# Kernel optimization log

Hardware: AMD Instinct MI355X
Metric: run time of the kernel (lower is better)

The kernel has to match this reference:

```python
import jax, jax.numpy as jnp
import numpy as np

B, H, S, DH = 2, 16, 2048, 64
MASK_FILL = -10000.0


def setup_inputs() -> dict:
    key = jax.random.key(0)
    kq, kk, kv = jax.random.split(key, 3)
    q = jax.random.normal(kq, (B, H, S, DH), dtype=jnp.float32)
    k = jax.random.normal(kk, (B, H, S, DH), dtype=jnp.float32)
    v = jax.random.normal(kv, (B, H, S, DH), dtype=jnp.float32)
    # causal mask: True where attention is disallowed (upper triangle)
    mask = jnp.triu(jnp.ones((S, S), dtype=jnp.bool_), k=1)
    return {"q": q, "k": k, "v": v, "mask": mask}


def reference(q, k, v, mask):
    scale = 1.0 / jnp.sqrt(jnp.asarray(k.shape[-1], dtype=q.dtype))
    # scores: [B, H, S_q, S_k]
    scores = jnp.einsum("bhqd,bhkd->bhqk", q, k) * scale
    # additive mask: masked_fill on a zeros [S_k, S_v] matrix -> -10000 where mask
    attn_bias = jnp.where(mask, jnp.asarray(MASK_FILL, dtype=k.dtype),
                          jnp.asarray(0.0, dtype=k.dtype))
    scores = scores + attn_bias  # broadcast over batch/heads
    attn = jax.nn.softmax(scores, axis=-1)
    # dropout_rate = 0.0 -> identity
    return jnp.einsum("bhqk,bhkd->bhqd", attn, v)
```

## Files before the change

kernel.cpp:

```cpp
#include <hip/hip_runtime.h>


#define S_LEN  2048
#define DHDIM  64
#define NHEADS 32
#define LDP    72
#define M2     23.083120654223414f
#define QSCALE 0.18033688011117658f

typedef __attribute__((ext_vector_type(8))) short bf16x8;
typedef __attribute__((ext_vector_type(4))) float f32x4;

__device__ __forceinline__ unsigned short f2bf(float f) {
    unsigned u = __float_as_uint(f);
    return (unsigned short)((u + 0x7fffu + ((u >> 16) & 1u)) >> 16);
}
__device__ __forceinline__ void ld8(const float* p, float* f) {
    float4 a = *(const float4*)p, b = *(const float4*)(p + 4);
    f[0]=a.x; f[1]=a.y; f[2]=a.z; f[3]=a.w; f[4]=b.x; f[5]=b.y; f[6]=b.z; f[7]=b.w;
}
__device__ __forceinline__ uint4 pack8(const float* f, float scale) {
    union { uint4 v; unsigned short s[8]; } w;
    #pragma unroll
    for (int j = 0; j < 8; j++) w.s[j] = f2bf(f[j] * scale);
    return w.v;
}
__device__ __forceinline__ unsigned packhi(float a, float b) {
#if __has_builtin(__builtin_amdgcn_perm)
    return __builtin_amdgcn_perm(__float_as_uint(b), __float_as_uint(a), 0x07060302u);
#else
    return (__float_as_uint(a) >> 16) | (__float_as_uint(b) & 0xffff0000u);
#endif
}

__global__ __launch_bounds__(256) void prep(
    const float* __restrict__ Qf, const float* __restrict__ Kf,
    const float* __restrict__ Vf, unsigned short* __restrict__ qb,
    unsigned short* __restrict__ kb, unsigned short* __restrict__ vtb)
{
    const int st = blockIdx.x, bh = blockIdx.y;
    __shared__ unsigned short lt[64][LDP];
    const float* vp = Vf + ((size_t)bh * S_LEN + st * 64) * DHDIM;
    for (int c = threadIdx.x; c < 512; c += 256) {
        int s = c >> 3, d0 = (c & 7) * 8;
        float f[8]; ld8(vp + s * DHDIM + d0, f);
        #pragma unroll
        for (int j = 0; j < 8; j++) lt[d0 + j][s] = f2bf(f[j]);
    }
    size_t off = ((size_t)(bh * 32 + st) * 4096) + (size_t)threadIdx.x * 16;
    float f[8];
    ld8(Qf + off, f);     *(uint4*)(qb + off)     = pack8(f, QSCALE);
    ld8(Qf + off + 8, f); *(uint4*)(qb + off + 8) = pack8(f, QSCALE);
    ld8(Kf + off, f);     *(uint4*)(kb + off)     = pack8(f, 1.0f);
    ld8(Kf + off + 8, f); *(uint4*)(kb + off + 8) = pack8(f, 1.0f);
    __syncthreads();
    unsigned short* op = vtb + (size_t)bh * DHDIM * S_LEN + st * 64;
    for (int c = threadIdx.x; c < 512; c += 256) {
        int d = c >> 3, s0 = (c & 7) * 8;
        *(uint4*)(op + (size_t)d * S_LEN + s0) = *(const uint4*)&lt[d][s0];
    }
}

__global__ __launch_bounds__(256) void fattn_splitk(
    const unsigned short* __restrict__ Qp, const unsigned short* __restrict__ Kp,
    const unsigned short* __restrict__ Vp,
    float* __restrict__ pO, float* __restrict__ pL)
{
    __shared__ unsigned short smem[192 * LDP];
    unsigned short (*ks)[LDP]  = (unsigned short(*)[LDP])smem;
    unsigned short (*vts)[LDP] = (unsigned short(*)[LDP])(smem + 64 * LDP);
    unsigned short (*qs)[LDP]  = (unsigned short(*)[LDP])(smem + 128 * LDP);
    unsigned short (*pst)[LDP] = qs;

    const int id   = blockIdx.y * 64 + blockIdx.x;
    const int qt   = 31 - (id >> 6);
    const int rem  = id & 63;
    const int bh   = rem >> 1;
    const int half = rem & 1;
    const int kmid = (qt + 2) >> 1;
    const int k0   = half ? kmid : 0;
    const int k1   = half ? qt + 1 : kmid;
    const int slot = ((bh * 32 + qt) << 1) | half;

    const int tid = threadIdx.x;
    const int wave = tid >> 6, lane = tid & 63;
    const int quad = lane >> 4, l16 = lane & 15;

    {
        const unsigned short* src = Qp + ((size_t)bh * S_LEN + qt * 64) * DHDIM;
        for (int c = tid; c < 512; c += 256) {
            int row = c >> 3, c8 = (c & 7) * 8;
            *(uint4*)&qs[row][c8] = *(const uint4*)(src + row * DHDIM + c8);
        }
    }
    __syncthreads();

    const int prow = wave * 16 + l16;
    const bf16x8 bq0 = *(const bf16x8*)&qs[prow][quad * 8];
    const bf16x8 bq1 = *(const bf16x8*)&qs[prow][32 + quad * 8];

    float l_p = 0.f;
    f32x4 of[4];
    #pragma unroll
    for (int n = 0; n < 4; n++) of[n] = (f32x4){0.f, 0.f, 0.f, 0.f};

    for (int kt = k0; kt < k1; kt++) {
        __syncthreads();

        const unsigned short* ksrc = Kp + ((size_t)bh * S_LEN + kt * 64) * DHDIM;
        const unsigned short* vsrc = Vp + (size_t)bh * DHDIM * S_LEN + kt * 64;
        for (int c = tid; c < 512; c += 256) {
            int row = c >> 3, c8 = (c & 7) * 8;
            *(uint4*)&ks[row][c8]  = *(const uint4*)(ksrc + row * DHDIM + c8);
            *(uint4*)&vts[row][c8] = *(const uint4*)(vsrc + (size_t)row * S_LEN + c8);
        }
        __syncthreads();

        f32x4 sf[4];
        #pragma unroll
        for (int n = 0; n < 4; n++) {
            bf16x8 ak0 = *(const bf16x8*)&ks[n * 16 + l16][quad * 8];
            bf16x8 ak1 = *(const bf16x8*)&ks[n * 16 + l16][32 + quad * 8];
            sf[n] = (f32x4){-M2, -M2, -M2, -M2};
            sf[n] = __builtin_amdgcn_mfma_f32_16x16x32_bf16(ak0, bq0, sf[n], 0, 0, 0);
            sf[n] = __builtin_amdgcn_mfma_f32_16x16x32_bf16(ak1, bq1, sf[n], 0, 0, 0);
        }

        const bool diag = (kt == qt);
        #pragma unroll
        for (int n = 0; n < 4; n++) {
            float p[4];
            #pragma unroll
            for (int r = 0; r < 4; r++) {
                p[r] = exp2f(sf[n][r]);
                if (diag && (n * 16 + quad * 4 + r > prow)) p[r] = 0.f;
                l_p += p[r];
            }
            uint2 dw;
            dw.x = packhi(p[0], p[1]);
            dw.y = packhi(p[2], p[3]);
            *(uint2*)&pst[prow][n * 16 + quad * 4] = dw;
        }
        asm volatile("s_waitcnt lgkmcnt(0)" ::: "memory");

        bf16x8 bp0 = *(const bf16x8*)&pst[prow][quad * 8];
        bf16x8 bp1 = *(const bf16x8*)&pst[prow][32 + quad * 8];
        #pragma unroll
        for (int n = 0; n < 4; n++) {
            bf16x8 av0 = *(const bf16x8*)&vts[n * 16 + l16][quad * 8];
            bf16x8 av1 = *(const bf16x8*)&vts[n * 16 + l16][32 + quad * 8];
            of[n] = __builtin_amdgcn_mfma_f32_16x16x32_bf16(av0, bp0, of[n], 0, 0, 0);
            of[n] = __builtin_amdgcn_mfma_f32_16x16x32_bf16(av1, bp1, of[n], 0, 0, 0);
        }
    }

    l_p += __shfl_xor(l_p, 16);
    l_p += __shfl_xor(l_p, 32);
    if (quad == 0) pL[slot * 64 + prow] = l_p;
    float* op = pO + (size_t)slot * 4096 + prow * 64;
    #pragma unroll
    for (int n = 0; n < 4; n++)
        *(float4*)(op + n * 16 + quad * 4) =
            make_float4(of[n][0], of[n][1], of[n][2], of[n][3]);
}

__global__ __launch_bounds__(256) void combine(
    const float* __restrict__ pO, const float* __restrict__ pL,
    float* __restrict__ O)
{
    const int qt = blockIdx.x, bh = blockIdx.y;
    const int sa = ((bh * 32 + qt) << 1), sb = sa | 1;
    const float* A = pO + (size_t)sa * 4096;
    const float* B = pO + (size_t)sb * 4096;
    float* out = O + ((size_t)bh * S_LEN + qt * 64) * DHDIM;
    #pragma unroll
    for (int k = 0; k < 4; k++) {
        int c = threadIdx.x + k * 256;
        int row = c >> 4;
        float inv = 1.f / (pL[sa * 64 + row] + pL[sb * 64 + row]);
        float4 a = *(const float4*)(A + c * 4);
        float4 b = *(const float4*)(B + c * 4);
        *(float4*)(out + c * 4) = make_float4(
            (a.x + b.x) * inv, (a.y + b.y) * inv,
            (a.z + b.z) * inv, (a.w + b.w) * inv);
    }
}

template <bool PRE>
__global__ __launch_bounds__(256) void fattn_kernel(
    const void* __restrict__ Qp, const void* __restrict__ Kp,
    const void* __restrict__ Vp, float* __restrict__ O)
{
    __shared__ unsigned short smem[192 * LDP];
    unsigned short (*ks)[LDP]  = (unsigned short(*)[LDP])smem;
    unsigned short (*vts)[LDP] = (unsigned short(*)[LDP])(smem + 64 * LDP);
    unsigned short (*qs)[LDP]  = (unsigned short(*)[LDP])(smem + 128 * LDP);
    unsigned short (*pst)[LDP] = qs;

    const int id = blockIdx.y * 32 + blockIdx.x;
    const int g  = id >> 8;
    const int r8 = id & 255;
    const int bh = r8 >> 3;
    const int s8 = r8 & 7;
    const int qt = (g == 0) ? 31 - 2 * s8 : (g == 1) ? 2 * s8
                 : (g == 2) ? 30 - 2 * s8 : 2 * s8 + 1;

    const int tid = threadIdx.x;
    const int wave = tid >> 6, lane = tid & 63;
    const int quad = lane >> 4, l16 = lane & 15;

    if constexpr (PRE) {
        const unsigned short* src = (const unsigned short*)Qp
            + ((size_t)bh * S_LEN + qt * 64) * DHDIM;
        for (int c = tid; c < 512; c += 256) {
            int row = c >> 3, c8 = (c & 7) * 8;
            *(uint4*)&qs[row][c8] = *(const uint4*)(src + row * DHDIM + c8);
        }
    } else {
        const float* src = (const float*)Qp + ((size_t)bh * S_LEN + qt * 64) * DHDIM;
        for (int c = tid; c < 512; c += 256) {
            int row = c >> 3, c8 = (c & 7) * 8;
            float f[8]; ld8(src + row * DHDIM + c8, f);
            *(uint4*)&qs[row][c8] = pack8(f, QSCALE);
        }
    }
    __syncthreads();

    const int prow = wave * 16 + l16;
    const bf16x8 bq0 = *(const bf16x8*)&qs[prow][quad * 8];
    const bf16x8 bq1 = *(const bf16x8*)&qs[prow][32 + quad * 8];

    float l_p = 0.f;
    f32x4 of[4];
    #pragma unroll
    for (int n = 0; n < 4; n++) of[n] = (f32x4){0.f, 0.f, 0.f, 0.f};

    for (int kt = 0; kt <= qt; kt++) {
        __syncthreads();
        if constexpr (PRE) {
            const unsigned short* ksrc = (const unsigned short*)Kp
                + ((size_t)bh * S_LEN + kt * 64) * DHDIM;
            const unsigned short* vsrc = (const unsigned short*)Vp
                + (size_t)bh * DHDIM * S_LEN + kt * 64;
            for (int c = tid; c < 512; c += 256) {
                int row = c >> 3, c8 = (c & 7) * 8;
                *(uint4*)&ks[row][c8]  = *(const uint4*)(ksrc + row * DHDIM + c8);
                *(uint4*)&vts[row][c8] = *(const uint4*)(vsrc + (size_t)row * S_LEN + c8);
            }
        } else {
            const float* ksrc = (const float*)Kp + ((size_t)bh * S_LEN + kt * 64) * DHDIM;
            const float* vsrc = (const float*)Vp + ((size_t)bh * S_LEN + kt * 64) * DHDIM;
            for (int c = tid; c < 512; c += 256) {
                int row = c >> 3, c8 = (c & 7) * 8;
                float f[8];
                ld8(ksrc + row * DHDIM + c8, f);
                *(uint4*)&ks[row][c8] = pack8(f, 1.0f);
                ld8(vsrc + row * DHDIM + c8, f);
                #pragma unroll
                for (int j = 0; j < 8; j++) vts[c8 + j][row] = f2bf(f[j]);
            }
        }
        __syncthreads();

        f32x4 sf[4];
        #pragma unroll
        for (int n = 0; n < 4; n++) {
            bf16x8 ak0 = *(const bf16x8*)&ks[n * 16 + l16][quad * 8];
            bf16x8 ak1 = *(const bf16x8*)&ks[n * 16 + l16][32 + quad * 8];
            sf[n] = (f32x4){-M2, -M2, -M2, -M2};
            sf[n] = __builtin_amdgcn_mfma_f32_16x16x32_bf16(ak0, bq0, sf[n], 0, 0, 0);
            sf[n] = __builtin_amdgcn_mfma_f32_16x16x32_bf16(ak1, bq1, sf[n], 0, 0, 0);
        }

        const bool diag = (kt == qt);
        #pragma unroll
        for (int n = 0; n < 4; n++) {
            float p[4];
            #pragma unroll
            for (int r = 0; r < 4; r++) {
                p[r] = exp2f(sf[n][r]);
                if (diag && (n * 16 + quad * 4 + r > prow)) p[r] = 0.f;
                l_p += p[r];
            }
            uint2 dw;
            dw.x = packhi(p[0], p[1]);
            dw.y = packhi(p[2], p[3]);
            *(uint2*)&pst[prow][n * 16 + quad * 4] = dw;
        }
        asm volatile("s_waitcnt lgkmcnt(0)" ::: "memory");

        bf16x8 bp0 = *(const bf16x8*)&pst[prow][quad * 8];
        bf16x8 bp1 = *(const bf16x8*)&pst[prow][32 + quad * 8];
        #pragma unroll
        for (int n = 0; n < 4; n++) {
            bf16x8 av0 = *(const bf16x8*)&vts[n * 16 + l16][quad * 8];
            bf16x8 av1 = *(const bf16x8*)&vts[n * 16 + l16][32 + quad * 8];
            of[n] = __builtin_amdgcn_mfma_f32_16x16x32_bf16(av0, bp0, of[n], 0, 0, 0);
            of[n] = __builtin_amdgcn_mfma_f32_16x16x32_bf16(av1, bp1, of[n], 0, 0, 0);
        }
    }

    l_p += __shfl_xor(l_p, 16);
    l_p += __shfl_xor(l_p, 32);
    const float inv = 1.f / l_p;
    float* op = O + ((size_t)bh * S_LEN + qt * 64 + prow) * DHDIM;
    #pragma unroll
    for (int n = 0; n < 4; n++)
        *(float4*)(op + n * 16 + quad * 4) = make_float4(
            of[n][0] * inv, of[n][1] * inv, of[n][2] * inv, of[n][3] * inv);
}

extern "C" void kernel_launch(void* const* d_in, const int* in_sizes, int n_in,
                              void* d_out, int out_size, void* d_ws, size_t ws_size,
                              hipStream_t stream) {
    const float* Q = (const float*)d_in[0];
    const float* K = (const float*)d_in[1];
    const float* V = (const float*)d_in[2];
    float* O = (float*)d_out;
    const size_t N = (size_t)NHEADS * S_LEN * DHDIM;
    const size_t prepB  = 3 * N * sizeof(unsigned short);
    const size_t partB  = (size_t)2048 * (4096 + 64) * sizeof(float);

    if (d_ws && ws_size >= prepB + partB) {
        unsigned short* qb  = (unsigned short*)d_ws;
        unsigned short* kb  = qb + N;
        unsigned short* vtb = kb + N;
        float* pO = (float*)((char*)d_ws + prepB);
        float* pL = pO + (size_t)2048 * 4096;
        prep<<<dim3(S_LEN / 64, NHEADS), 256, 0, stream>>>(Q, K, V, qb, kb, vtb);
        fattn_splitk<<<dim3(64, 32), 256, 0, stream>>>(qb, kb, vtb, pO, pL);
        combine<<<dim3(32, 32), 256, 0, stream>>>(pO, pL, O);
    } else if (d_ws && ws_size >= prepB) {
        unsigned short* qb  = (unsigned short*)d_ws;
        unsigned short* kb  = qb + N;
        unsigned short* vtb = kb + N;
        prep<<<dim3(S_LEN / 64, NHEADS), 256, 0, stream>>>(Q, K, V, qb, kb, vtb);
        fattn_kernel<true><<<dim3(32, 32), 256, 0, stream>>>(qb, kb, vtb, O);
    } else {
        fattn_kernel<false><<<dim3(32, 32), 256, 0, stream>>>(Q, K, V, O);
    }
}
```

Baseline: 149.3 us.

## Fuse split-K combine into attention via atomic pairing, MFMA row sums, swizzled transpose

Removes the separate combine kernel. The second of each pair of split-K blocks to finish waits on a ready flag and merges the partial output directly, and the flags are reset inside the prep kernel. The row sum of P is now computed with an extra MFMA against a ones vector instead of scalar adds and shuffles. Two further changes: exp2f is replaced by the hardware exp2 builtin, and the V transpose in prep uses an XOR-swizzled LDS layout to avoid bank conflicts. The spin-wait depends on the partner block being resident or already finished, which adds a risk of stalls.

```diff
diff --git a/kernel.cpp b/kernel.cpp
--- a/kernel.cpp
+++ b/kernel.cpp
@@ -11,6 +11,13 @@
 typedef __attribute__((ext_vector_type(8))) short bf16x8;
 typedef __attribute__((ext_vector_type(4))) float f32x4;
 
+__device__ __forceinline__ float fast_exp2(float x) {
+#if __has_builtin(__builtin_amdgcn_exp2f)
+    return __builtin_amdgcn_exp2f(x);
+#else
+    return exp2f(x);
+#endif
+}
 __device__ __forceinline__ unsigned short f2bf(float f) {
     unsigned u = __float_as_uint(f);
     return (unsigned short)((u + 0x7fffu + ((u >> 16) & 1u)) >> 16);
@@ -36,16 +43,23 @@
 __global__ __launch_bounds__(256) void prep(
     const float* __restrict__ Qf, const float* __restrict__ Kf,
     const float* __restrict__ Vf, unsigned short* __restrict__ qb,
-    unsigned short* __restrict__ kb, unsigned short* __restrict__ vtb)
+    unsigned short* __restrict__ kb, unsigned short* __restrict__ vtb,
+    int* __restrict__ flags)
 {
     const int st = blockIdx.x, bh = blockIdx.y;
+    if (flags && threadIdx.x < 2)
+        flags[threadIdx.x * 1024 + bh * 32 + st] = 0;
     __shared__ unsigned short lt[64][LDP];
     const float* vp = Vf + ((size_t)bh * S_LEN + st * 64) * DHDIM;
     for (int c = threadIdx.x; c < 512; c += 256) {
         int s = c >> 3, d0 = (c & 7) * 8;
         float f[8]; ld8(vp + s * DHDIM + d0, f);
         #pragma unroll
-        for (int j = 0; j < 8; j++) lt[d0 + j][s] = f2bf(f[j]);
+        for (int j = 0; j < 8; j++) {
+            int d = d0 + j;
+            int col = (s & 7) | ((((s >> 3) ^ (d >> 3)) & 7) << 3);
+            lt[d][col] = f2bf(f[j]);
+        }
     }
     size_t off = ((size_t)(bh * 32 + st) * 4096) + (size_t)threadIdx.x * 16;
     float f[8];
@@ -56,17 +70,20 @@
     __syncthreads();
     unsigned short* op = vtb + (size_t)bh * DHDIM * S_LEN + st * 64;
     for (int c = threadIdx.x; c < 512; c += 256) {
-        int d = c >> 3, s0 = (c & 7) * 8;
-        *(uint4*)(op + (size_t)d * S_LEN + s0) = *(const uint4*)&lt[d][s0];
+        int d = c >> 3, q = c & 7;
+        int colc = ((q ^ (d >> 3)) & 7) << 3;
+        *(uint4*)(op + (size_t)d * S_LEN + q * 8) = *(const uint4*)&lt[d][colc];
     }
 }
 
 __global__ __launch_bounds__(256) void fattn_splitk(
     const unsigned short* __restrict__ Qp, const unsigned short* __restrict__ Kp,
     const unsigned short* __restrict__ Vp,
-    float* __restrict__ pO, float* __restrict__ pL)
+    float* __restrict__ pO, float* __restrict__ pL,
+    int* __restrict__ flags, float* __restrict__ O)
 {
     __shared__ unsigned short smem[192 * LDP];
+    __shared__ int s_old;
     unsigned short (*ks)[LDP]  = (unsigned short(*)[LDP])smem;
     unsigned short (*vts)[LDP] = (unsigned short(*)[LDP])(smem + 64 * LDP);
     unsigned short (*qs)[LDP]  = (unsigned short(*)[LDP])(smem + 128 * LDP);
@@ -80,7 +97,8 @@
     const int kmid = (qt + 2) >> 1;
     const int k0   = half ? kmid : 0;
     const int k1   = half ? qt + 1 : kmid;
-    const int slot = ((bh * 32 + qt) << 1) | half;
+    const int pair = bh * 32 + qt;
+    const int slot = (pair << 1) | half;
 
     const int tid = threadIdx.x;
     const int wave = tid >> 6, lane = tid & 63;
@@ -99,8 +117,12 @@
     const bf16x8 bq0 = *(const bf16x8*)&qs[prow][quad * 8];
     const bf16x8 bq1 = *(const bf16x8*)&qs[prow][32 + quad * 8];
 
-    float l_p = 0.f;
+    bf16x8 ones;
+    #pragma unroll
+    for (int j = 0; j < 8; j++) ones[j] = (short)0x3F80;
+
     f32x4 of[4];
+    f32x4 of_l = (f32x4){0.f, 0.f, 0.f, 0.f};
     #pragma unroll
     for (int n = 0; n < 4; n++) of[n] = (f32x4){0.f, 0.f, 0.f, 0.f};
 
@@ -132,9 +154,8 @@
             float p[4];
             #pragma unroll
             for (int r = 0; r < 4; r++) {
-                p[r] = exp2f(sf[n][r]);
+                p[r] = fast_exp2(sf[n][r]);
                 if (diag && (n * 16 + quad * 4 + r > prow)) p[r] = 0.f;
-                l_p += p[r];
             }
             uint2 dw;
             dw.x = packhi(p[0], p[1]);
@@ -145,6 +166,8 @@
 
         bf16x8 bp0 = *(const bf16x8*)&pst[prow][quad * 8];
         bf16x8 bp1 = *(const bf16x8*)&pst[prow][32 + quad * 8];
+        of_l = __builtin_amdgcn_mfma_f32_16x16x32_bf16(ones, bp0, of_l, 0, 0, 0);
+        of_l = __builtin_amdgcn_mfma_f32_16x16x32_bf16(ones, bp1, of_l, 0, 0, 0);
         #pragma unroll
         for (int n = 0; n < 4; n++) {
             bf16x8 av0 = *(const bf16x8*)&vts[n * 16 + l16][quad * 8];
@@ -154,35 +177,42 @@
         }
     }
 
-    l_p += __shfl_xor(l_p, 16);
-    l_p += __shfl_xor(l_p, 32);
-    if (quad == 0) pL[slot * 64 + prow] = l_p;
-    float* op = pO + (size_t)slot * 4096 + prow * 64;
-    #pragma unroll
-    for (int n = 0; n < 4; n++)
-        *(float4*)(op + n * 16 + quad * 4) =
-            make_float4(of[n][0], of[n][1], of[n][2], of[n][3]);
-}
-
-__global__ __launch_bounds__(256) void combine(
-    const float* __restrict__ pO, const float* __restrict__ pL,
-    float* __restrict__ O)
-{
-    const int qt = blockIdx.x, bh = blockIdx.y;
-    const int sa = ((bh * 32 + qt) << 1), sb = sa | 1;
-    const float* A = pO + (size_t)sa * 4096;
-    const float* B = pO + (size_t)sb * 4096;
-    float* out = O + ((size_t)bh * S_LEN + qt * 64) * DHDIM;
-    #pragma unroll
-    for (int k = 0; k < 4; k++) {
-        int c = threadIdx.x + k * 256;
-        int row = c >> 4;
-        float inv = 1.f / (pL[sa * 64 + row] + pL[sb * 64 + row]);
-        float4 a = *(const float4*)(A + c * 4);
-        float4 b = *(const float4*)(B + c * 4);
-        *(float4*)(out + c * 4) = make_float4(
-            (a.x + b.x) * inv, (a.y + b.y) * inv,
-            (a.z + b.z) * inv, (a.w + b.w) * inv);
+    int* cnt = flags;
+    int* rdy = flags + 1024;
+    if (tid == 0) s_old = atomicAdd(&cnt[pair], 1);
+    __syncthreads();
+
+    if (s_old == 0) {
+        if (quad == 0) pL[slot * 64 + prow] = of_l[0];
+        float* op = pO + (size_t)slot * 4096 + prow * 64;
+        #pragma unroll
+        for (int n = 0; n < 4; n++)
+            *(float4*)(op + n * 16 + quad * 4) =
+                make_float4(of[n][0], of[n][1], of[n][2], of[n][3]);
+        __threadfence();
+        __syncthreads();
+        if (tid == 0)
+            __hip_atomic_store(&rdy[pair], 1, __ATOMIC_RELEASE,
+                               __HIP_MEMORY_SCOPE_AGENT);
+    } else {
+        if (tid == 0) {
+            while (__hip_atomic_load(&rdy[pair], __ATOMIC_ACQUIRE,
+                                     __HIP_MEMORY_SCOPE_AGENT) == 0)
+                __builtin_amdgcn_s_sleep(2);
+        }
+        __syncthreads();
+        __threadfence();
+        const int pslot = slot ^ 1;
+        const float inv = 1.f / (of_l[0] + pL[pslot * 64 + prow]);
+        const float* pp = pO + (size_t)pslot * 4096 + prow * 64;
+        float* op = O + ((size_t)bh * S_LEN + qt * 64 + prow) * DHDIM;
+        #pragma unroll
+        for (int n = 0; n < 4; n++) {
+            float4 a = *(const float4*)(pp + n * 16 + quad * 4);
+            *(float4*)(op + n * 16 + quad * 4) = make_float4(
+                (of[n][0] + a.x) * inv, (of[n][1] + a.y) * inv,
+                (of[n][2] + a.z) * inv, (of[n][3] + a.w) * inv);
+        }
     }
 }
 
@@ -278,7 +308,7 @@
             float p[4];
             #pragma unroll
             for (int r = 0; r < 4; r++) {
-                p[r] = exp2f(sf[n][r]);
+                p[r] = fast_exp2(sf[n][r]);
                 if (diag && (n * 16 + quad * 4 + r > prow)) p[r] = 0.f;
                 l_p += p[r];
             }
@@ -320,21 +350,22 @@
     const size_t N = (size_t)NHEADS * S_LEN * DHDIM;
     const size_t prepB  = 3 * N * sizeof(unsigned short);
     const size_t partB  = (size_t)2048 * (4096 + 64) * sizeof(float);
-
-    if (d_ws && ws_size >= prepB + partB) {
+    const size_t flagB  = 2048 * sizeof(int);
+
+    if (d_ws && ws_size >= prepB + partB + flagB) {
         unsigned short* qb  = (unsigned short*)d_ws;
         unsigned short* kb  = qb + N;
         unsigned short* vtb = kb + N;
         float* pO = (float*)((char*)d_ws + prepB);
         float* pL = pO + (size_t)2048 * 4096;
-        prep<<<dim3(S_LEN / 64, NHEADS), 256, 0, stream>>>(Q, K, V, qb, kb, vtb);
-        fattn_splitk<<<dim3(64, 32), 256, 0, stream>>>(qb, kb, vtb, pO, pL);
-        combine<<<dim3(32, 32), 256, 0, stream>>>(pO, pL, O);
+        int* flags = (int*)((char*)d_ws + prepB + partB);
+        prep<<<dim3(S_LEN / 64, NHEADS), 256, 0, stream>>>(Q, K, V, qb, kb, vtb, flags);
+        fattn_splitk<<<dim3(64, 32), 256, 0, stream>>>(qb, kb, vtb, pO, pL, flags, O);
     } else if (d_ws && ws_size >= prepB) {
         unsigned short* qb  = (unsigned short*)d_ws;
         unsigned short* kb  = qb + N;
         unsigned short* vtb = kb + N;
-        prep<<<dim3(S_LEN / 64, NHEADS), 256, 0, stream>>>(Q, K, V, qb, kb, vtb);
+        prep<<<dim3(S_LEN / 64, NHEADS), 256, 0, stream>>>(Q, K, V, qb, kb, vtb, nullptr);
         fattn_kernel<true><<<dim3(32, 32), 256, 0, stream>>>(qb, kb, vtb, O);
     } else {
         fattn_kernel<false><<<dim3(32, 32), 256, 0, stream>>>(Q, K, V, O);
```

After: 431.0 us. +188.6%, slower.

## Split only long query tiles, compute row sums via MFMA, swizzle transpose LDS

Applied to the files above, without the earlier changes.

The split-K attention now splits only query tiles 16-31 into two halves. Short tiles are processed whole and written straight to the output, and a constant table orders the work blocks from longest to shortest. The softmax denominator is accumulated with an extra MFMA against a ones vector instead of scalar adds and cross-lane shuffles, and exp2 uses the hardware builtin. The prep kernel's V transpose uses an XOR-swizzled LDS layout to reduce bank conflicts. Together these cut the number of combine tiles and the partial-result traffic, at the cost of table-driven scheduling and an extra MFMA per tile.

```diff
diff --git a/kernel.cpp b/kernel.cpp
--- a/kernel.cpp
+++ b/kernel.cpp
@@ -11,6 +11,26 @@
 typedef __attribute__((ext_vector_type(8))) short bf16x8;
 typedef __attribute__((ext_vector_type(4))) float f32x4;
 
+__device__ __constant__ unsigned char T_QT[48] = {
+    31,31,30,15, 30,29,29,28,14, 28,27,27,26,13, 26,25,25,24,12,
+    24,23,23,22,11, 22,21,21,20,10, 20,19,19,18,9, 18,17,17,16,8,
+    16,7, 6,5,4,3,2,1,0};
+__device__ __constant__ unsigned char T_K0[48] = {
+    0,16,0,0, 16,0,15,0,0, 15,0,14,0,0, 14,0,13,0,0,
+    13,0,12,0,0, 12,0,11,0,0, 11,0,10,0,0, 10,0,9,0,0,
+    9,0, 0,0,0,0,0,0,0};
+__device__ __constant__ unsigned char T_K1[48] = {
+    16,32,16,16, 31,15,30,15,15, 29,14,28,14,14, 27,13,26,13,13,
+    25,12,24,12,12, 23,11,22,11,11, 21,10,20,10,10, 19,9,18,9,9,
+    17,8, 7,6,5,4,3,2,1};
+
+__device__ __forceinline__ float fast_exp2(float x) {
+#if __has_builtin(__builtin_amdgcn_exp2f)
+    return __builtin_amdgcn_exp2f(x);
+#else
+    return exp2f(x);
+#endif
+}
 __device__ __forceinline__ unsigned short f2bf(float f) {
     unsigned u = __float_as_uint(f);
     return (unsigned short)((u + 0x7fffu + ((u >> 16) & 1u)) >> 16);
@@ -45,7 +65,11 @@
         int s = c >> 3, d0 = (c & 7) * 8;
         float f[8]; ld8(vp + s * DHDIM + d0, f);
         #pragma unroll
-        for (int j = 0; j < 8; j++) lt[d0 + j][s] = f2bf(f[j]);
+        for (int j = 0; j < 8; j++) {
+            int d = d0 + j;
+            int col = (s & 7) | ((((s >> 3) ^ (d >> 3)) & 7) << 3);
+            lt[d][col] = f2bf(f[j]);
+        }
     }
     size_t off = ((size_t)(bh * 32 + st) * 4096) + (size_t)threadIdx.x * 16;
     float f[8];
@@ -56,15 +80,16 @@
     __syncthreads();
     unsigned short* op = vtb + (size_t)bh * DHDIM * S_LEN + st * 64;
     for (int c = threadIdx.x; c < 512; c += 256) {
-        int d = c >> 3, s0 = (c & 7) * 8;
-        *(uint4*)(op + (size_t)d * S_LEN + s0) = *(const uint4*)&lt[d][s0];
+        int d = c >> 3, q = c & 7;
+        int colc = ((q ^ (d >> 3)) & 7) << 3;
+        *(uint4*)(op + (size_t)d * S_LEN + q * 8) = *(const uint4*)&lt[d][colc];
     }
 }
 
 __global__ __launch_bounds__(256) void fattn_splitk(
     const unsigned short* __restrict__ Qp, const unsigned short* __restrict__ Kp,
     const unsigned short* __restrict__ Vp,
-    float* __restrict__ pO, float* __restrict__ pL)
+    float* __restrict__ pO, float* __restrict__ pL, float* __restrict__ O)
 {
     __shared__ unsigned short smem[192 * LDP];
     unsigned short (*ks)[LDP]  = (unsigned short(*)[LDP])smem;
@@ -72,15 +97,12 @@
     unsigned short (*qs)[LDP]  = (unsigned short(*)[LDP])(smem + 128 * LDP);
     unsigned short (*pst)[LDP] = qs;
 
-    const int id   = blockIdx.y * 64 + blockIdx.x;
-    const int qt   = 31 - (id >> 6);
-    const int rem  = id & 63;
-    const int bh   = rem >> 1;
-    const int half = rem & 1;
-    const int kmid = (qt + 2) >> 1;
-    const int k0   = half ? kmid : 0;
-    const int k1   = half ? qt + 1 : kmid;
-    const int slot = ((bh * 32 + qt) << 1) | half;
+    const int bh   = blockIdx.x;
+    const int rank = blockIdx.y;
+    const int qt   = T_QT[rank];
+    const int k0   = T_K0[rank];
+    const int k1   = T_K1[rank];
+    const bool whole = (k1 - k0 == qt + 1);
 
     const int tid = threadIdx.x;
     const int wave = tid >> 6, lane = tid & 63;
@@ -99,8 +121,12 @@
     const bf16x8 bq0 = *(const bf16x8*)&qs[prow][quad * 8];
     const bf16x8 bq1 = *(const bf16x8*)&qs[prow][32 + quad * 8];
 
-    float l_p = 0.f;
+    bf16x8 ones;
+    #pragma unroll
+    for (int j = 0; j < 8; j++) ones[j] = (short)0x3F80;
+
     f32x4 of[4];
+    f32x4 of_l = (f32x4){0.f, 0.f, 0.f, 0.f};
     #pragma unroll
     for (int n = 0; n < 4; n++) of[n] = (f32x4){0.f, 0.f, 0.f, 0.f};
 
@@ -132,9 +158,8 @@
             float p[4];
             #pragma unroll
             for (int r = 0; r < 4; r++) {
-                p[r] = exp2f(sf[n][r]);
+                p[r] = fast_exp2(sf[n][r]);
                 if (diag && (n * 16 + quad * 4 + r > prow)) p[r] = 0.f;
-                l_p += p[r];
             }
             uint2 dw;
             dw.x = packhi(p[0], p[1]);
@@ -145,6 +170,8 @@
 
         bf16x8 bp0 = *(const bf16x8*)&pst[prow][quad * 8];
         bf16x8 bp1 = *(const bf16x8*)&pst[prow][32 + quad * 8];
+        of_l = __builtin_amdgcn_mfma_f32_16x16x32_bf16(ones, bp0, of_l, 0, 0, 0);
+        of_l = __builtin_amdgcn_mfma_f32_16x16x32_bf16(ones, bp1, of_l, 0, 0, 0);
         #pragma unroll
         for (int n = 0; n < 4; n++) {
             bf16x8 av0 = *(const bf16x8*)&vts[n * 16 + l16][quad * 8];
@@ -154,22 +181,30 @@
         }
     }
 
-    l_p += __shfl_xor(l_p, 16);
-    l_p += __shfl_xor(l_p, 32);
-    if (quad == 0) pL[slot * 64 + prow] = l_p;
-    float* op = pO + (size_t)slot * 4096 + prow * 64;
-    #pragma unroll
-    for (int n = 0; n < 4; n++)
-        *(float4*)(op + n * 16 + quad * 4) =
-            make_float4(of[n][0], of[n][1], of[n][2], of[n][3]);
+    if (whole) {
+        const float inv = 1.f / of_l[0];
+        float* op = O + ((size_t)bh * S_LEN + qt * 64 + prow) * DHDIM;
+        #pragma unroll
+        for (int n = 0; n < 4; n++)
+            *(float4*)(op + n * 16 + quad * 4) = make_float4(
+                of[n][0] * inv, of[n][1] * inv, of[n][2] * inv, of[n][3] * inv);
+    } else {
+        const int slot = ((bh * 16 + (qt - 16)) << 1) | (k0 != 0 ? 1 : 0);
+        if (quad == 0) pL[slot * 64 + prow] = of_l[0];
+        float* op = pO + (size_t)slot * 4096 + prow * 64;
+        #pragma unroll
+        for (int n = 0; n < 4; n++)
+            *(float4*)(op + n * 16 + quad * 4) =
+                make_float4(of[n][0], of[n][1], of[n][2], of[n][3]);
+    }
 }
 
 __global__ __launch_bounds__(256) void combine(
     const float* __restrict__ pO, const float* __restrict__ pL,
     float* __restrict__ O)
 {
-    const int qt = blockIdx.x, bh = blockIdx.y;
-    const int sa = ((bh * 32 + qt) << 1), sb = sa | 1;
+    const int qt = 16 + blockIdx.x, bh = blockIdx.y;
+    const int sa = ((bh * 16 + (qt - 16)) << 1), sb = sa | 1;
     const float* A = pO + (size_t)sa * 4096;
     const float* B = pO + (size_t)sb * 4096;
     float* out = O + ((size_t)bh * S_LEN + qt * 64) * DHDIM;
@@ -278,7 +313,7 @@
             float p[4];
             #pragma unroll
             for (int r = 0; r < 4; r++) {
-                p[r] = exp2f(sf[n][r]);
+                p[r] = fast_exp2(sf[n][r]);
                 if (diag && (n * 16 + quad * 4 + r > prow)) p[r] = 0.f;
                 l_p += p[r];
             }
@@ -319,17 +354,17 @@
     float* O = (float*)d_out;
     const size_t N = (size_t)NHEADS * S_LEN * DHDIM;
     const size_t prepB  = 3 * N * sizeof(unsigned short);
-    const size_t partB  = (size_t)2048 * (4096 + 64) * sizeof(float);
+    const size_t partB  = (size_t)1024 * (4096 + 64) * sizeof(float);
 
     if (d_ws && ws_size >= prepB + partB) {
         unsigned short* qb  = (unsigned short*)d_ws;
         unsigned short* kb  = qb + N;
         unsigned short* vtb = kb + N;
         float* pO = (float*)((char*)d_ws + prepB);
-        float* pL = pO + (size_t)2048 * 4096;
+        float* pL = pO + (size_t)1024 * 4096;
         prep<<<dim3(S_LEN / 64, NHEADS), 256, 0, stream>>>(Q, K, V, qb, kb, vtb);
-        fattn_splitk<<<dim3(64, 32), 256, 0, stream>>>(qb, kb, vtb, pO, pL);
-        combine<<<dim3(32, 32), 256, 0, stream>>>(pO, pL, O);
+        fattn_splitk<<<dim3(32, 48), 256, 0, stream>>>(qb, kb, vtb, pO, pL, O);
+        combine<<<dim3(16, 32), 256, 0, stream>>>(pO, pL, O);
     } else if (d_ws && ws_size >= prepB) {
         unsigned short* qb  = (unsigned short*)d_ws;
         unsigned short* kb  = qb + N;
```

Result: faster. 144.8 us (-3.1%).
